# Kernel tuning notes

Hardware: AMD Instinct MI355X
Metric: run time of the kernel (lower is better)

## Reference

```python
import jax, jax.numpy as jnp
import numpy as np

B, N, DIM, H, DK, DV = 2, 2048, 1536, 8, 64, 192


def relative_shift(x):
    # x: [b, h, t1, 2*t1-1] -> [b, h, t1, t1] via Transformer-XL pad/reshape trick
    b, h, t1, t2 = x.shape
    x = jnp.pad(x, ((0, 0), (0, 0), (0, 0), (1, 0)))  # prepend zero column
    t2p = t2 + 1
    x = x.reshape(b, h, t2p, t1)
    x = x[:, :, 1:, :].reshape(b, h, t1, t2)
    return x[..., : (t2p + 1) // 2]


def setup_inputs() -> dict:
    key = jax.random.key(0)
    ks = jax.random.split(key, 9)
    s = 0.02
    return {
        "x": jax.random.normal(ks[0], (B, N, DIM), jnp.float32),
        "Wq": jax.random.normal(ks[1], (DIM, H * DK), jnp.float32) * s,
        "Wk": jax.random.normal(ks[2], (DIM, H * DK), jnp.float32) * s,
        "Wv": jax.random.normal(ks[3], (DIM, H * DV), jnp.float32) * s,
        "W_rel": jax.random.normal(ks[4], (1, H * DK), jnp.float32) * s,
        "Wo": jax.random.normal(ks[5], (H * DV, DIM), jnp.float32) * s,
        "bo": jnp.zeros((DIM,), jnp.float32),
        "rel_content_bias": jax.random.normal(ks[6], (1, H, 1, DK), jnp.float32),
        "rel_pos_bias": jax.random.normal(ks[7], (1, H, 1, DK), jnp.float32),
    }


def reference(x, Wq, Wk, Wv, W_rel, Wo, bo, rel_content_bias, rel_pos_bias):
    b, n, _ = x.shape
    scale = DK ** -0.5
    split = lambda t, d: t.reshape(b, n, H, d).transpose(0, 2, 1, 3)  # b h n d
    q = split(x @ Wq, DK) * scale
    k = split(x @ Wk, DK)
    v = split(x @ Wv, DV)

    content_logits = jnp.einsum("bhid,bhjd->bhij", q + rel_content_bias, k)

    distances = jnp.arange(-n + 1, n, dtype=jnp.float32)[:, None]  # [2n-1, 1]
    rel_k = (distances @ W_rel).reshape(2 * n - 1, H, DK).transpose(1, 0, 2)  # h j d
    rel_logits = jnp.einsum("bhid,hjd->bhij", q + rel_pos_bias, rel_k)
    rel_logits = relative_shift(rel_logits)

    attn = jax.nn.softmax(content_logits + rel_logits, axis=-1)
    out = jnp.einsum("bhij,bhjd->bhid", attn, v)
    out = out.transpose(0, 2, 1, 3).reshape(b, n, H * DV)
    return out @ Wo + bo
```

## Files before the change

kernel.cpp:

```cpp
#include <hip/hip_runtime.h>
#include <math.h>

typedef __attribute__((ext_vector_type(8))) short short8;
typedef __attribute__((ext_vector_type(4))) float floatx4;

namespace {
constexpr int kB = 2, kN = 2048, kDIM = 1536, kH = 8, kDK = 64, kDV = 192;
constexpr int kHDV = kH * kDV;
constexpr float kScale = 0.125f;
constexpr float kLog2e = 1.44269504088896340736f;
}

__device__ __forceinline__ unsigned short f2b(float f) {
    union { float f; unsigned u; } v; v.f = f;
    unsigned r = (v.u + 0x7FFFu + ((v.u >> 16) & 1u)) >> 16;
    return (unsigned short)r;
}

__global__ __launch_bounds__(256) void conv_w(
    const float* __restrict__ src, unsigned short* __restrict__ dst, int Ncols)
{
    __shared__ float Ts[32][33];
    const int tx = threadIdx.x & 31, ty = threadIdx.x >> 5;
    const int k0 = blockIdx.x * 32, n0 = blockIdx.y * 32;
#pragma unroll
    for (int p = 0; p < 4; ++p)
        Ts[ty + p * 8][tx] = src[(size_t)(k0 + ty + p * 8) * Ncols + n0 + tx];
    __syncthreads();
#pragma unroll
    for (int p = 0; p < 4; ++p)
        dst[(size_t)(n0 + ty + p * 8) * kDIM + k0 + tx] = f2b(Ts[tx][ty + p * 8]);
}

__global__ __launch_bounds__(256) void conv_x(
    const float* __restrict__ x, unsigned short* __restrict__ xb)
{
    int idx = blockIdx.x * 256 + threadIdx.x;
    float4 v = *(const float4*)&x[(size_t)idx * 4];
    ushort4 o; o.x = f2b(v.x); o.y = f2b(v.y); o.z = f2b(v.z); o.w = f2b(v.w);
    *(ushort4*)&xb[(size_t)idx * 4] = o;
}

__global__ __launch_bounds__(256) void wcm_pre(
    const float* __restrict__ Wq, const float* __restrict__ Wrel,
    const float* __restrict__ rpb, float* __restrict__ wcm)
{
    int gid = blockIdx.x * 256 + threadIdx.x;
    if (gid < 12288) {
        int dim = gid >> 3, h = gid & 7;
        float s = 0.f;
#pragma unroll 8
        for (int d = 0; d < 64; ++d)
            s += Wq[(size_t)dim * 512 + h * 64 + d] * Wrel[h * 64 + d];
        wcm[h * kDIM + dim] = s * kScale * kLog2e;
    } else if (gid < 12296) {
        int h = gid - 12288;
        float s = 0.f;
#pragma unroll 8
        for (int d = 0; d < 64; ++d) s += rpb[h * 64 + d] * Wrel[h * 64 + d];
        wcm[12288 + h] = s * kLog2e;
    }
}

__global__ __launch_bounds__(256) void c_gemm(
    const float* __restrict__ x, const float* __restrict__ wcm,
    float* __restrict__ cw)
{
    const int row  = blockIdx.x * 4 + (threadIdx.x >> 6);
    const int lane = threadIdx.x & 63;
    const float* xr = x + (size_t)row * kDIM;

    float4 xv[6];
#pragma unroll
    for (int c = 0; c < 6; ++c)
        xv[c] = *(const float4*)&xr[c * 256 + lane * 4];

    float acc[8];
#pragma unroll
    for (int h = 0; h < 8; ++h) {
        const float* wr = wcm + h * kDIM;
        float a = 0.f;
#pragma unroll
        for (int c = 0; c < 6; ++c) {
            float4 wv = *(const float4*)&wr[c * 256 + lane * 4];
            a += xv[c].x * wv.x + xv[c].y * wv.y + xv[c].z * wv.z + xv[c].w * wv.w;
        }
        acc[h] = a;
    }
#pragma unroll
    for (int h = 0; h < 8; ++h) {
        float a = acc[h];
        a += __shfl_xor(a, 1, 64);
        a += __shfl_xor(a, 2, 64);
        a += __shfl_xor(a, 4, 64);
        a += __shfl_xor(a, 8, 64);
        a += __shfl_xor(a, 16, 64);
        a += __shfl_xor(a, 32, 64);
        acc[h] = a;
    }
    if (lane == 0) {
        const int b = row >> 11, i = row & 2047;
#pragma unroll
        for (int h = 0; h < 8; ++h)
            cw[(size_t)(b * 8 + h) * kN + i] = acc[h] + wcm[12288 + h];
    }
}

__global__ __launch_bounds__(256) void mm_qkv(
    const unsigned short* __restrict__ xb,
    const unsigned short* __restrict__ wt,
    const float* __restrict__ rcb,
    unsigned short* __restrict__ qo,
    unsigned short* __restrict__ ko,
    unsigned short* __restrict__ vo)
{
    __shared__ unsigned short A_lds[128 * 72];
    __shared__ unsigned short B_lds[128 * 72];
    const int tid = threadIdx.x;
    const int wave = tid >> 6, lane = tid & 63, lm = lane & 15, lg = lane >> 4;
    const int bm = blockIdx.y * 128, bn = blockIdx.x * 128;
    const int mb = (wave >> 1) * 64, nb = (wave & 1) * 64;

    floatx4 acc[4][4];
#pragma unroll
    for (int i = 0; i < 4; ++i)
#pragma unroll
        for (int j = 0; j < 4; ++j)
#pragma unroll
            for (int r = 0; r < 4; ++r) acc[i][j][r] = 0.f;

    const int srow = tid >> 3, scc = (tid & 7) * 8;
    short8 ra[4], rb[4];
#pragma unroll
    for (int p = 0; p < 4; ++p) {
        ra[p] = *(const short8*)&xb[(size_t)(bm + srow + p * 32) * kDIM + scc];
        rb[p] = *(const short8*)&wt[(size_t)(bn + srow + p * 32) * kDIM + scc];
    }

    for (int kt = 0; kt < 24; ++kt) {
        __syncthreads();
#pragma unroll
        for (int p = 0; p < 4; ++p) {
            *(short8*)&A_lds[(srow + p * 32) * 72 + scc] = ra[p];
            *(short8*)&B_lds[(srow + p * 32) * 72 + scc] = rb[p];
        }
        __syncthreads();
        if (kt < 23) {
            int k0 = (kt + 1) * 64;
#pragma unroll
            for (int p = 0; p < 4; ++p) {
                ra[p] = *(const short8*)&xb[(size_t)(bm + srow + p * 32) * kDIM + k0 + scc];
                rb[p] = *(const short8*)&wt[(size_t)(bn + srow + p * 32) * kDIM + k0 + scc];
            }
        }
#pragma unroll
        for (int ks = 0; ks < 2; ++ks) {
            short8 af[4], bf[4];
#pragma unroll
            for (int mi = 0; mi < 4; ++mi)
                af[mi] = *(const short8*)&A_lds[(mb + mi * 16 + lm) * 72 + lg * 8 + 32 * ks];
#pragma unroll
            for (int ni = 0; ni < 4; ++ni)
                bf[ni] = *(const short8*)&B_lds[(nb + ni * 16 + lm) * 72 + lg * 8 + 32 * ks];
#pragma unroll
            for (int mi = 0; mi < 4; ++mi)
#pragma unroll
                for (int ni = 0; ni < 4; ++ni)
                    acc[mi][ni] = __builtin_amdgcn_mfma_f32_16x16x32_bf16(
                        af[mi], bf[ni], acc[mi][ni], 0, 0, 0);
        }
    }

#pragma unroll
    for (int mi = 0; mi < 4; ++mi)
#pragma unroll
        for (int ni = 0; ni < 4; ++ni)
#pragma unroll
            for (int r = 0; r < 4; ++r) {
                int row = bm + mb + mi * 16 + lg * 4 + r;
                int b = row >> 11, i = row & 2047;
                int col = bn + nb + ni * 16 + lm;
                float v = acc[mi][ni][r];
                if (bn < 512) {
                    int h = col >> 6, d = col & 63;
                    qo[((size_t)(b * 8 + h) * kN + i) * kDK + d] =
                        f2b((v * kScale + rcb[h * 64 + d]) * kLog2e);
                } else if (bn < 1024) {
                    int c2 = col - 512, h = c2 >> 6, d = c2 & 63;
                    ko[((size_t)(b * 8 + h) * kN + i) * kDK + d] = f2b(v);
                } else {
                    int c2 = col - 1024, h = c2 / 192, d = c2 - h * 192;
                    vo[((size_t)(b * 8 + h) * kN + i) * kDV + d] = f2b(v);
                }
            }
}

__global__ __launch_bounds__(256) void vtrans(
    const unsigned short* __restrict__ vw, unsigned short* __restrict__ vt)
{
    __shared__ unsigned short Ts[32][33];
    const int tx = threadIdx.x & 31, ty = threadIdx.x >> 5;
    const int i0 = blockIdx.x * 32, d0 = blockIdx.y * 32, bh = blockIdx.z;
#pragma unroll
    for (int p = 0; p < 4; ++p)
        Ts[ty + p * 8][tx] = vw[((size_t)bh * kN + i0 + ty + p * 8) * kDV + d0 + tx];
    __syncthreads();
#pragma unroll
    for (int p = 0; p < 4; ++p)
        vt[((size_t)bh * kDV + d0 + ty + p * 8) * kN + i0 + tx] = Ts[tx][ty + p * 8];
}

__global__ __launch_bounds__(256) void flash_attn(
    const unsigned short* __restrict__ q,
    const unsigned short* __restrict__ k,
    const unsigned short* __restrict__ vt,
    const float* __restrict__ crel,
    unsigned short* __restrict__ ao)
{
    __shared__ unsigned short K_lds[64 * 72];
    __shared__ unsigned short V_lds[192 * 72];
    __shared__ unsigned short P_lds[4 * 16 * 68];
    __shared__ float cs[64];

    const int tid = threadIdx.x;
    const int wave = tid >> 6, lane = tid & 63, lm = lane & 15, lg = lane >> 4;
    const int id = blockIdx.x;
    const int rem = id >> 3;
    const int bh = (id & 7) * 2 + (rem >> 5);
    const int i0 = (rem & 31) * 64;

    short8 qA[2];
    {
        const size_t qb = ((size_t)bh * kN + i0 + wave * 16 + lm) * kDK + lg * 8;
        qA[0] = *(const short8*)&q[qb];
        qA[1] = *(const short8*)&q[qb + 32];
    }
    if (tid < 64) cs[tid] = crel[(size_t)bh * kN + i0 + tid];

    floatx4 o4[12];
#pragma unroll
    for (int nd = 0; nd < 12; ++nd)
#pragma unroll
        for (int r = 0; r < 4; ++r) o4[nd][r] = 0.f;
    float m_[4] = {-INFINITY, -INFINITY, -INFINITY, -INFINITY};
    float l_[4] = {0.f, 0.f, 0.f, 0.f};

    const unsigned short* kb = k + (size_t)bh * kN * kDK;
    const unsigned short* vb = vt + (size_t)bh * kDV * kN;
    const int pbase = wave * 16 * 68;
    const int srow = tid >> 3, scol = (tid & 7) * 8;

    short8 rk[2], rv[6];
#pragma unroll
    for (int p = 0; p < 2; ++p)
        rk[p] = *(const short8*)&kb[(size_t)(srow + p * 32) * kDK + scol];
#pragma unroll
    for (int p = 0; p < 6; ++p)
        rv[p] = *(const short8*)&vb[(size_t)(srow + p * 32) * kN + scol];

    for (int t = 0; t < 32; ++t) {
        const int j0 = t * 64;
        __syncthreads();
#pragma unroll
        for (int p = 0; p < 2; ++p)
            *(short8*)&K_lds[(srow + p * 32) * 72 + scol] = rk[p];
#pragma unroll
        for (int p = 0; p < 6; ++p)
            *(short8*)&V_lds[(srow + p * 32) * 72 + scol] = rv[p];
        __syncthreads();
        if (t < 31) {
            const int j1 = j0 + 64;
#pragma unroll
            for (int p = 0; p < 2; ++p)
                rk[p] = *(const short8*)&kb[(size_t)(j1 + srow + p * 32) * kDK + scol];
#pragma unroll
            for (int p = 0; p < 6; ++p)
                rv[p] = *(const short8*)&vb[(size_t)(srow + p * 32) * kN + j1 + scol];
        }

        floatx4 s4[4];
#pragma unroll
        for (int st = 0; st < 4; ++st) {
#pragma unroll
            for (int r = 0; r < 4; ++r) s4[st][r] = 0.f;
#pragma unroll
            for (int ks = 0; ks < 2; ++ks) {
                short8 kf = *(const short8*)&K_lds[(st * 16 + lm) * 72 + lg * 8 + 32 * ks];
                s4[st] = __builtin_amdgcn_mfma_f32_16x16x32_bf16(qA[ks], kf, s4[st], 0, 0, 0);
            }
        }

        float alpha[4];
#pragma unroll
        for (int r = 0; r < 4; ++r) {
            const int row = wave * 16 + lg * 4 + r;
            const float ci = cs[row];
            const float gi = (float)(i0 + row);
            float sv[4];
#pragma unroll
            for (int st = 0; st < 4; ++st)
                sv[st] = s4[st][r] + ((float)(j0 + st * 16 + lm) - gi) * ci;
            float mx = fmaxf(fmaxf(sv[0], sv[1]), fmaxf(sv[2], sv[3]));
            mx = fmaxf(mx, __shfl_xor(mx, 1, 64));
            mx = fmaxf(mx, __shfl_xor(mx, 2, 64));
            mx = fmaxf(mx, __shfl_xor(mx, 4, 64));
            mx = fmaxf(mx, __shfl_xor(mx, 8, 64));
            float mnew = fmaxf(m_[r], mx);
            alpha[r] = exp2f(m_[r] - mnew);
            m_[r] = mnew;
            float ts = 0.f;
#pragma unroll
            for (int st = 0; st < 4; ++st) {
                float pv = exp2f(sv[st] - mnew);
                ts += pv;
                P_lds[pbase + (lg * 4 + r) * 68 + st * 16 + lm] = f2b(pv);
            }
            ts += __shfl_xor(ts, 1, 64);
            ts += __shfl_xor(ts, 2, 64);
            ts += __shfl_xor(ts, 4, 64);
            ts += __shfl_xor(ts, 8, 64);
            l_[r] = l_[r] * alpha[r] + ts;
        }

#pragma unroll
        for (int nd = 0; nd < 12; ++nd)
#pragma unroll
            for (int r = 0; r < 4; ++r) o4[nd][r] *= alpha[r];

        short8 pa[2];
        pa[0] = *(const short8*)&P_lds[pbase + lm * 68 + lg * 8];
        pa[1] = *(const short8*)&P_lds[pbase + lm * 68 + lg * 8 + 32];
#pragma unroll
        for (int nd = 0; nd < 12; ++nd) {
#pragma unroll
            for (int ks = 0; ks < 2; ++ks) {
                short8 vf = *(const short8*)&V_lds[(nd * 16 + lm) * 72 + lg * 8 + 32 * ks];
                o4[nd] = __builtin_amdgcn_mfma_f32_16x16x32_bf16(pa[ks], vf, o4[nd], 0, 0, 0);
            }
        }
    }

    const int b = bh >> 3, h = bh & 7;
#pragma unroll
    for (int r = 0; r < 4; ++r) {
        float inv = 1.f / l_[r];
        size_t rowbase = ((size_t)b * kN + i0 + wave * 16 + lg * 4 + r) * (size_t)kHDV
                         + h * kDV;
#pragma unroll
        for (int nd = 0; nd < 12; ++nd)
            ao[rowbase + nd * 16 + lm] = f2b(o4[nd][r] * inv);
    }
}

__global__ __launch_bounds__(256) void mm_out(
    const unsigned short* __restrict__ aw,
    const unsigned short* __restrict__ wot,
    const float* __restrict__ bias,
    float* __restrict__ out)
{
    __shared__ unsigned short A_lds[128 * 72];
    __shared__ unsigned short B_lds[128 * 72];
    const int tid = threadIdx.x;
    const int wave = tid >> 6, lane = tid & 63, lm = lane & 15, lg = lane >> 4;
    const int bm = blockIdx.y * 128, bn = blockIdx.x * 128;
    const int mb = (wave >> 1) * 64, nb = (wave & 1) * 64;

    floatx4 acc[4][4];
#pragma unroll
    for (int i = 0; i < 4; ++i)
#pragma unroll
        for (int j = 0; j < 4; ++j)
#pragma unroll
            for (int r = 0; r < 4; ++r) acc[i][j][r] = 0.f;

    const int srow = tid >> 3, scc = (tid & 7) * 8;
    short8 ra[4], rb[4];
#pragma unroll
    for (int p = 0; p < 4; ++p) {
        ra[p] = *(const short8*)&aw[(size_t)(bm + srow + p * 32) * kDIM + scc];
        rb[p] = *(const short8*)&wot[(size_t)(bn + srow + p * 32) * kDIM + scc];
    }

    for (int kt = 0; kt < 24; ++kt) {
        __syncthreads();
#pragma unroll
        for (int p = 0; p < 4; ++p) {
            *(short8*)&A_lds[(srow + p * 32) * 72 + scc] = ra[p];
            *(short8*)&B_lds[(srow + p * 32) * 72 + scc] = rb[p];
        }
        __syncthreads();
        if (kt < 23) {
            int k0 = (kt + 1) * 64;
#pragma unroll
            for (int p = 0; p < 4; ++p) {
                ra[p] = *(const short8*)&aw[(size_t)(bm + srow + p * 32) * kDIM + k0 + scc];
                rb[p] = *(const short8*)&wot[(size_t)(bn + srow + p * 32) * kDIM + k0 + scc];
            }
        }
#pragma unroll
        for (int ks = 0; ks < 2; ++ks) {
            short8 af[4], bf[4];
#pragma unroll
            for (int mi = 0; mi < 4; ++mi)
                af[mi] = *(const short8*)&A_lds[(mb + mi * 16 + lm) * 72 + lg * 8 + 32 * ks];
#pragma unroll
            for (int ni = 0; ni < 4; ++ni)
                bf[ni] = *(const short8*)&B_lds[(nb + ni * 16 + lm) * 72 + lg * 8 + 32 * ks];
#pragma unroll
            for (int mi = 0; mi < 4; ++mi)
#pragma unroll
                for (int ni = 0; ni < 4; ++ni)
                    acc[mi][ni] = __builtin_amdgcn_mfma_f32_16x16x32_bf16(
                        af[mi], bf[ni], acc[mi][ni], 0, 0, 0);
        }
    }

#pragma unroll
    for (int mi = 0; mi < 4; ++mi)
#pragma unroll
        for (int ni = 0; ni < 4; ++ni)
#pragma unroll
            for (int r = 0; r < 4; ++r) {
                int row = bm + mb + mi * 16 + lg * 4 + r;
                int col = bn + nb + ni * 16 + lm;
                out[(size_t)row * kDIM + col] = acc[mi][ni][r] + bias[col];
            }
}

extern "C" void kernel_launch(void* const* d_in, const int* in_sizes, int n_in,
                              void* d_out, int out_size, void* d_ws, size_t ws_size,
                              hipStream_t stream)
{
    const float* x    = (const float*)d_in[0];
    const float* Wq   = (const float*)d_in[1];
    const float* Wk   = (const float*)d_in[2];
    const float* Wv   = (const float*)d_in[3];
    const float* Wrel = (const float*)d_in[4];
    const float* Wo   = (const float*)d_in[5];
    const float* bo   = (const float*)d_in[6];
    const float* rcb  = (const float*)d_in[7];
    const float* rpb  = (const float*)d_in[8];
    float* out = (float*)d_out;

    char* w = (char*)d_ws;
    unsigned short* xb  = (unsigned short*)(w);
    unsigned short* wt  = (unsigned short*)(w + 12582912);
    unsigned short* qw  = (unsigned short*)(w + 20447232);
    unsigned short* kw  = (unsigned short*)(w + 24641536);
    unsigned short* vw  = (unsigned short*)(w + 28835840);
    float*          cw  = (float*)(w + 41418752);
    float*          wcm = (float*)(w + 41549824);
    unsigned short* vtp = xb;
    unsigned short* awp = vw;
    unsigned short* wot = wt;

    { dim3 g(48, 16);  conv_w<<<g, 256, 0, stream>>>(Wq, wt,               512); }
    { dim3 g(48, 16);  conv_w<<<g, 256, 0, stream>>>(Wk, wt + 512  * 1536, 512); }
    { dim3 g(48, 48);  conv_w<<<g, 256, 0, stream>>>(Wv, wt + 1024 * 1536, 1536); }
    conv_x<<<6144, 256, 0, stream>>>(x, xb);
    wcm_pre<<<49, 256, 0, stream>>>(Wq, Wrel, rpb, wcm);
    c_gemm<<<1024, 256, 0, stream>>>(x, wcm, cw);

    { dim3 g(20, 32); mm_qkv<<<g, 256, 0, stream>>>(xb, wt, rcb, qw, kw, vw); }

    { dim3 g(48, 48); conv_w<<<g, 256, 0, stream>>>(Wo, wot, 1536); }
    { dim3 g(64, 6, 16); vtrans<<<g, 256, 0, stream>>>(vw, vtp); }

    flash_attn<<<512, 256, 0, stream>>>(qw, kw, vtp, cw, awp);

    { dim3 g(12, 32); mm_out<<<g, 256, 0, stream>>>(awp, wot, bo, out); }
}
```

Before: 339.4 us.

## Use lazy softmax rescaling and MFMA row sums, drop register prefetch in flash attention

The online softmax now skips the cross-lane max reduction and the rescale of the output accumulators unless some row's new max exceeds the running max by more than 8 (in log2 units), and it computes row sums with an MFMA against a ones vector instead of shuffle reductions. The rel-pos bias term is folded into a single FMA with precomputed per-row constants held in registers, and the probabilities use cheaper round-half-up bf16 conversion. The register-staged prefetch of the next K/V tile is removed, so global loads now go directly to LDS each iteration. This cuts VALU and shuffle work in the softmax, but it adds load latency that is no longer overlapped, and with lazy rescaling the exponentials can reach up to 2^8.

```diff
diff --git a/kernel.cpp b/kernel.cpp
--- a/kernel.cpp
+++ b/kernel.cpp
@@ -15,6 +15,10 @@
     union { float f; unsigned u; } v; v.f = f;
     unsigned r = (v.u + 0x7FFFu + ((v.u >> 16) & 1u)) >> 16;
     return (unsigned short)r;
+}
+__device__ __forceinline__ unsigned short f2b_fast(float f) {
+    union { float f; unsigned u; } v; v.f = f;
+    return (unsigned short)((v.u + 0x8000u) >> 16);
 }
 
 __global__ __launch_bounds__(256) void conv_w(
@@ -220,7 +224,6 @@
     __shared__ unsigned short K_lds[64 * 72];
     __shared__ unsigned short V_lds[192 * 72];
     __shared__ unsigned short P_lds[4 * 16 * 68];
-    __shared__ float cs[64];
 
     const int tid = threadIdx.x;
     const int wave = tid >> 6, lane = tid & 63, lm = lane & 15, lg = lane >> 4;
@@ -235,48 +238,45 @@
         qA[0] = *(const short8*)&q[qb];
         qA[1] = *(const short8*)&q[qb + 32];
     }
-    if (tid < 64) cs[tid] = crel[(size_t)bh * kN + i0 + tid];
+    float cR[4], gici[4];
+#pragma unroll
+    for (int r = 0; r < 4; ++r) {
+        const int row = wave * 16 + lg * 4 + r;
+        cR[r]   = crel[(size_t)bh * kN + i0 + row];
+        gici[r] = (float)(i0 + row) * cR[r];
+    }
 
     floatx4 o4[12];
 #pragma unroll
     for (int nd = 0; nd < 12; ++nd)
 #pragma unroll
         for (int r = 0; r < 4; ++r) o4[nd][r] = 0.f;
+    floatx4 lacc;
+#pragma unroll
+    for (int r = 0; r < 4; ++r) lacc[r] = 0.f;
     float m_[4] = {-INFINITY, -INFINITY, -INFINITY, -INFINITY};
-    float l_[4] = {0.f, 0.f, 0.f, 0.f};
 
     const unsigned short* kb = k + (size_t)bh * kN * kDK;
     const unsigned short* vb = vt + (size_t)bh * kDV * kN;
     const int pbase = wave * 16 * 68;
     const int srow = tid >> 3, scol = (tid & 7) * 8;
 
-    short8 rk[2], rv[6];
-#pragma unroll
-    for (int p = 0; p < 2; ++p)
-        rk[p] = *(const short8*)&kb[(size_t)(srow + p * 32) * kDK + scol];
-#pragma unroll
-    for (int p = 0; p < 6; ++p)
-        rv[p] = *(const short8*)&vb[(size_t)(srow + p * 32) * kN + scol];
+    short8 ones;
+#pragma unroll
+    for (int u = 0; u < 8; ++u) ones[u] = (short)0x3F80;
 
     for (int t = 0; t < 32; ++t) {
         const int j0 = t * 64;
         __syncthreads();
 #pragma unroll
         for (int p = 0; p < 2; ++p)
-            *(short8*)&K_lds[(srow + p * 32) * 72 + scol] = rk[p];
+            *(short8*)&K_lds[(srow + p * 32) * 72 + scol] =
+                *(const short8*)&kb[(size_t)(j0 + srow + p * 32) * kDK + scol];
 #pragma unroll
         for (int p = 0; p < 6; ++p)
-            *(short8*)&V_lds[(srow + p * 32) * 72 + scol] = rv[p];
-        __syncthreads();
-        if (t < 31) {
-            const int j1 = j0 + 64;
-#pragma unroll
-            for (int p = 0; p < 2; ++p)
-                rk[p] = *(const short8*)&kb[(size_t)(j1 + srow + p * 32) * kDK + scol];
-#pragma unroll
-            for (int p = 0; p < 6; ++p)
-                rv[p] = *(const short8*)&vb[(size_t)(srow + p * 32) * kN + j1 + scol];
-        }
+            *(short8*)&V_lds[(srow + p * 32) * 72 + scol] =
+                *(const short8*)&vb[(size_t)(srow + p * 32) * kN + j0 + scol];
+        __syncthreads();
 
         floatx4 s4[4];
 #pragma unroll
@@ -290,46 +290,50 @@
             }
         }
 
-        float alpha[4];
-#pragma unroll
-        for (int r = 0; r < 4; ++r) {
-            const int row = wave * 16 + lg * 4 + r;
-            const float ci = cs[row];
-            const float gi = (float)(i0 + row);
-            float sv[4];
-#pragma unroll
-            for (int st = 0; st < 4; ++st)
-                sv[st] = s4[st][r] + ((float)(j0 + st * 16 + lm) - gi) * ci;
-            float mx = fmaxf(fmaxf(sv[0], sv[1]), fmaxf(sv[2], sv[3]));
-            mx = fmaxf(mx, __shfl_xor(mx, 1, 64));
-            mx = fmaxf(mx, __shfl_xor(mx, 2, 64));
-            mx = fmaxf(mx, __shfl_xor(mx, 4, 64));
-            mx = fmaxf(mx, __shfl_xor(mx, 8, 64));
-            float mnew = fmaxf(m_[r], mx);
-            alpha[r] = exp2f(m_[r] - mnew);
-            m_[r] = mnew;
-            float ts = 0.f;
-#pragma unroll
-            for (int st = 0; st < 4; ++st) {
-                float pv = exp2f(sv[st] - mnew);
-                ts += pv;
-                P_lds[pbase + (lg * 4 + r) * 68 + st * 16 + lm] = f2b(pv);
-            }
-            ts += __shfl_xor(ts, 1, 64);
-            ts += __shfl_xor(ts, 2, 64);
-            ts += __shfl_xor(ts, 4, 64);
-            ts += __shfl_xor(ts, 8, 64);
-            l_[r] = l_[r] * alpha[r] + ts;
-        }
-
-#pragma unroll
-        for (int nd = 0; nd < 12; ++nd)
-#pragma unroll
-            for (int r = 0; r < 4; ++r) o4[nd][r] *= alpha[r];
+        float sv[4][4];
+        float lmax[4];
+#pragma unroll
+        for (int r = 0; r < 4; ++r) lmax[r] = -INFINITY;
+#pragma unroll
+        for (int st = 0; st < 4; ++st) {
+            const float jf = (float)(j0 + st * 16 + lm);
+#pragma unroll
+            for (int r = 0; r < 4; ++r) {
+                float v = fmaf(jf, cR[r], s4[st][r] - gici[r]);
+                sv[st][r] = v;
+                lmax[r] = fmaxf(lmax[r], v);
+            }
+        }
+        bool ok = (lmax[0] <= m_[0] + 8.f) && (lmax[1] <= m_[1] + 8.f) &&
+                  (lmax[2] <= m_[2] + 8.f) && (lmax[3] <= m_[3] + 8.f);
+        if (!__all(ok)) {
+#pragma unroll
+            for (int r = 0; r < 4; ++r) {
+                float mx = lmax[r];
+                mx = fmaxf(mx, __shfl_xor(mx, 1, 64));
+                mx = fmaxf(mx, __shfl_xor(mx, 2, 64));
+                mx = fmaxf(mx, __shfl_xor(mx, 4, 64));
+                mx = fmaxf(mx, __shfl_xor(mx, 8, 64));
+                float mnew = fmaxf(m_[r], mx);
+                float alpha = exp2f(m_[r] - mnew);
+                m_[r] = mnew;
+                lacc[r] *= alpha;
+#pragma unroll
+                for (int nd = 0; nd < 12; ++nd) o4[nd][r] *= alpha;
+            }
+        }
+#pragma unroll
+        for (int st = 0; st < 4; ++st)
+#pragma unroll
+            for (int r = 0; r < 4; ++r)
+                P_lds[pbase + (lg * 4 + r) * 68 + st * 16 + lm] =
+                    f2b_fast(exp2f(sv[st][r] - m_[r]));
 
         short8 pa[2];
         pa[0] = *(const short8*)&P_lds[pbase + lm * 68 + lg * 8];
         pa[1] = *(const short8*)&P_lds[pbase + lm * 68 + lg * 8 + 32];
+        lacc = __builtin_amdgcn_mfma_f32_16x16x32_bf16(pa[0], ones, lacc, 0, 0, 0);
+        lacc = __builtin_amdgcn_mfma_f32_16x16x32_bf16(pa[1], ones, lacc, 0, 0, 0);
 #pragma unroll
         for (int nd = 0; nd < 12; ++nd) {
 #pragma unroll
@@ -343,7 +347,7 @@
     const int b = bh >> 3, h = bh & 7;
 #pragma unroll
     for (int r = 0; r < 4; ++r) {
-        float inv = 1.f / l_[r];
+        float inv = 1.f / lacc[r];
         size_t rowbase = ((size_t)b * kN + i0 + wave * 16 + lg * 4 + r) * (size_t)kHDV
                          + h * kDV;
 #pragma unroll
```

New measurement: 329.4 us. -3.0%, faster.
